# Kernel tuning notes

Measured on AMD Instinct MI355X. Metric: run time of the kernel, lower is better.

Reference implementation:

```python
import jax, jax.numpy as jnp
import numpy as np

B, N, D, H = 4, 2048, 512, 8
DH = D // H
EPS = 1e-6


def setup_inputs() -> dict:
    key = jax.random.key(0)
    ks = jax.random.split(key, 12)
    s = 1.0 / np.sqrt(D)
    return {
        "x": jax.random.normal(ks[0], (B, N, D), jnp.float32),
        "attn_bias": jax.random.normal(ks[1], (B, 1, N, N), jnp.float32),
        "Wq": jax.random.normal(ks[2], (D, D), jnp.float32) * s,
        "bq": jnp.zeros((D,), jnp.float32),
        "Wk": jax.random.normal(ks[3], (D, D), jnp.float32) * s,
        "bk": jnp.zeros((D,), jnp.float32),
        "Wv": jax.random.normal(ks[4], (D, D), jnp.float32) * s,
        "bv": jnp.zeros((D,), jnp.float32),
        "Wo": jax.random.normal(ks[5], (D, D), jnp.float32) * s,
        "bo": jnp.zeros((D,), jnp.float32),
        "q_gamma": jnp.ones((DH,), jnp.float32),
        "q_beta": jnp.zeros((DH,), jnp.float32),
        "k_gamma": jnp.ones((DH,), jnp.float32),
        "k_beta": jnp.zeros((DH,), jnp.float32),
    }


def _layernorm(x, gamma, beta):
    mu = jnp.mean(x, axis=-1, keepdims=True)
    var = jnp.var(x, axis=-1, keepdims=True)
    return (x - mu) * jax.lax.rsqrt(var + EPS) * gamma + beta


def reference(x, attn_bias, Wq, bq, Wk, bk, Wv, bv, Wo, bo,
              q_gamma, q_beta, k_gamma, k_beta):
    b, n, d = x.shape
    # project and split heads: (B, H, N, DH)
    def heads(W, bias):
        return (x @ W.T + bias).reshape(b, n, H, DH).transpose(0, 2, 1, 3)
    q = heads(Wq, bq)
    k = heads(Wk, bk)
    v = heads(Wv, bv)
    q = _layernorm(q, q_gamma, q_beta)
    k = _layernorm(k, k_gamma, k_beta)
    scores = jnp.einsum('bhqd,bhkd->bhqk', q, k) / np.sqrt(DH)
    scores = scores + attn_bias  # (B,1,N,N) broadcasts over heads
    attn = jax.nn.softmax(scores, axis=-1)
    out = jnp.einsum('bhqk,bhkd->bhqd', attn, v)
    out = out.transpose(0, 2, 1, 3).reshape(b, n, d)
    return out @ Wo.T + bo
```

## Files before the change

### kernel.cpp

```cpp
#include <hip/hip_runtime.h>

typedef __attribute__((ext_vector_type(8))) short short8;
typedef __attribute__((ext_vector_type(4))) float f32x4;
typedef __attribute__((ext_vector_type(4))) int i32x4;
typedef __attribute__((ext_vector_type(4))) unsigned short u16x4;
typedef __attribute__((ext_vector_type(2))) unsigned int u32x2;

#define B_  4
#define N_  2048
#define D_  512
#define H_  8
#define DH_ 64
#define M_  (B_ * N_)

__device__ __forceinline__ unsigned short f2bf(float f) {
    union { float f; unsigned u; } un; un.f = f;
    unsigned r = un.u + 0x7FFFu + ((un.u >> 16) & 1u);
    return (unsigned short)(r >> 16);
}
__device__ __forceinline__ float exp2fast(float x) {
#if __has_builtin(__builtin_amdgcn_exp2f)
    return __builtin_amdgcn_exp2f(x);
#else
    float r; asm("v_exp_f32 %0, %1" : "=v"(r) : "v"(x)); return r;
#endif
}
__device__ __forceinline__ unsigned cvtpk_bf16(float lo, float hi) {
    unsigned r;
    asm("v_cvt_pk_bf16_f32 %0, %1, %2" : "=v"(r) : "v"(lo), "v"(hi));
    return r;
}
__device__ __forceinline__ float max3f(float a, float b, float c) {
    return fmaxf(fmaxf(a, b), c);
}

typedef __attribute__((address_space(1))) const void gvoid;
typedef __attribute__((address_space(3))) void svoid;
__device__ __forceinline__ void load16_lds(const void* g, void* s) {
    __builtin_amdgcn_global_load_lds((gvoid*)g, (svoid*)s, 16, 0, 0);
}

__global__ __launch_bounds__(256) void cvt_all(
    const float* __restrict__ x,
    const float* __restrict__ W0, const float* __restrict__ W1,
    const float* __restrict__ W2, const float* __restrict__ W3,
    unsigned short* __restrict__ xb, unsigned short* __restrict__ Wb) {
    const int bx = blockIdx.x;
    const float* src;
    unsigned short* dst;
    int i;
    if (bx < 4096) {
        src = x; dst = xb;
        i = (bx * 256 + (int)threadIdx.x) * 4;
    } else {
        const int r = bx - 4096;
        const int sel = r >> 8;
        src = (sel == 0) ? W0 : (sel == 1) ? W1 : (sel == 2) ? W2 : W3;
        dst = Wb + (size_t)sel * D_ * D_;
        i = ((r & 255) * 256 + (int)threadIdx.x) * 4;
    }
    f32x4 v = *(const f32x4*)(src + i);
    u16x4 o;
    o[0] = f2bf(v[0]); o[1] = f2bf(v[1]); o[2] = f2bf(v[2]); o[3] = f2bf(v[3]);
    *(u16x4*)(dst + i) = o;
}

template <bool F32OUT, bool LNF>
__global__ __launch_bounds__(256, 2) void gemm_nt(
    const unsigned short* __restrict__ A,
    const unsigned short* __restrict__ W,
    const float* __restrict__ Bv0,
    const float* __restrict__ Bv1,
    const float* __restrict__ Bv2,
    const float* __restrict__ g0, const float* __restrict__ be0,
    const float* __restrict__ g1, const float* __restrict__ be1,
    unsigned short* __restrict__ outb,
    float* __restrict__ outf)
{
    const int mt = blockIdx.x;
    const int nt = blockIdx.y;
    const int sel = nt >> 2;
    const unsigned short* Wp = W + (size_t)sel * D_ * D_;
    const float* Bv = (sel == 0) ? Bv0 : (sel == 1) ? Bv1 : Bv2;
    const int n0 = (nt & 3) * 128;

    __shared__ __align__(16) unsigned short As[128 * 32];
    __shared__ __align__(16) unsigned short Bs[128 * 32];

    const int tid = threadIdx.x;
    const int w   = tid >> 6;
    const int l   = tid & 63;
    const int l15 = l & 15;
    const int qd  = l >> 4;
    const int wr  = w >> 1;
    const int wc  = w & 1;

    int srow[2], scol[2];
#pragma unroll
    for (int c = 0; c < 2; ++c) {
        const int g   = (w * 2 + c) * 64 + l;
        const int row = g >> 2;
        srow[c] = row;
        scol[c] = ((g & 3) ^ (row & 3)) * 8;
    }

    f32x4 acc[4][4];
#pragma unroll
    for (int i = 0; i < 4; ++i)
#pragma unroll
        for (int j = 0; j < 4; ++j)
            acc[i][j] = (f32x4){0.f, 0.f, 0.f, 0.f};

    const int swz = qd ^ (l15 & 3);

    for (int k0 = 0; k0 < D_; k0 += 32) {
        __syncthreads();
#pragma unroll
        for (int c = 0; c < 2; ++c) {
            load16_lds(A  + (size_t)(mt * 128 + srow[c]) * D_ + k0 + scol[c],
                       As + (w * 2 + c) * 512);
            load16_lds(Wp + (size_t)(n0 + srow[c]) * D_ + k0 + scol[c],
                       Bs + (w * 2 + c) * 512);
        }
        __syncthreads();

        short8 af[4], bfr[4];
#pragma unroll
        for (int rt = 0; rt < 4; ++rt)
            af[rt] = *(const short8*)&As[(wr * 64 + rt * 16 + l15) * 32 + swz * 8];
#pragma unroll
        for (int ct = 0; ct < 4; ++ct)
            bfr[ct] = *(const short8*)&Bs[(wc * 64 + ct * 16 + l15) * 32 + swz * 8];
#pragma unroll
        for (int rt = 0; rt < 4; ++rt)
#pragma unroll
            for (int ct = 0; ct < 4; ++ct)
                acc[rt][ct] = __builtin_amdgcn_mfma_f32_16x16x32_bf16(
                    af[rt], bfr[ct], acc[rt][ct], 0, 0, 0);
    }

    const float* gam = (sel == 0) ? g0 : g1;
    const float* bet = (sel == 0) ? be0 : be1;
    float gv[4], bv2[4];
    if (LNF) {
#pragma unroll
        for (int ct = 0; ct < 4; ++ct) { gv[ct] = gam[ct * 16 + l15]; bv2[ct] = bet[ct * 16 + l15]; }
    }

#pragma unroll
    for (int rt = 0; rt < 4; ++rt) {
        float v[4][4];
#pragma unroll
        for (int ct = 0; ct < 4; ++ct) {
            const float bias = Bv[n0 + wc * 64 + ct * 16 + l15];
#pragma unroll
            for (int r = 0; r < 4; ++r) v[ct][r] = acc[rt][ct][r] + bias;
        }
        if (LNF && sel < 2) {
#pragma unroll
            for (int r = 0; r < 4; ++r) {
                float s  = v[0][r] + v[1][r] + v[2][r] + v[3][r];
                float s2 = v[0][r]*v[0][r] + v[1][r]*v[1][r] + v[2][r]*v[2][r] + v[3][r]*v[3][r];
#pragma unroll
                for (int o = 1; o <= 8; o <<= 1) {
                    s  += __shfl_xor(s, o);
                    s2 += __shfl_xor(s2, o);
                }
                const float mu  = s * 0.015625f;
                const float var = s2 * 0.015625f - mu * mu;
                const float rs  = rsqrtf(var + 1e-6f);
#pragma unroll
                for (int ct = 0; ct < 4; ++ct)
                    v[ct][r] = (v[ct][r] - mu) * rs * gv[ct] + bv2[ct];
            }
        }
#pragma unroll
        for (int ct = 0; ct < 4; ++ct) {
            const int col  = n0 + wc * 64 + ct * 16 + l15;
            const int row0 = mt * 128 + wr * 64 + rt * 16 + qd * 4;
#pragma unroll
            for (int r = 0; r < 4; ++r) {
                const size_t oidx = (size_t)(row0 + r) * D_ + col;
                if (F32OUT) outf[oidx] = v[ct][r];
                else        outb[(size_t)sel * M_ * D_ + oidx] = f2bf(v[ct][r]);
            }
        }
    }
}

__global__ __launch_bounds__(256) void pack_kv(
    const unsigned short* __restrict__ K, const unsigned short* __restrict__ V,
    unsigned short* __restrict__ Kt, unsigned short* __restrict__ Vt2)
{
    const int nt = blockIdx.x, b = blockIdx.y;
    const int tid = threadIdx.x;
    __shared__ __align__(16) unsigned short Vl[64][520];

#pragma unroll
    for (int i = 0; i < 16; ++i) {
        const int c = i * 256 + tid;
        const int row = c >> 6, ch = c & 63;
        const size_t srow = ((size_t)(b * N_ + nt * 64 + row)) * D_ + ch * 8;
        i32x4 kd = *(const i32x4*)(K + srow);
        const int h = ch >> 3, dc = ch & 7;
        *(i32x4*)(Kt + ((((size_t)(b * 8 + h) * 32 + nt) * 64 + row) * 64) + dc * 8) = kd;
        i32x4 vd = *(const i32x4*)(V + srow);
        *(i32x4*)&Vl[row][ch * 8] = vd;
    }
    __syncthreads();
#pragma unroll
    for (int i = 0; i < 16; ++i) {
        const int c = i * 256 + tid;
        const int h = c >> 9, r = c & 511;
        const int dh = r >> 3, kc = r & 7;
        u16x4 o0, o1;
#pragma unroll
        for (int j = 0; j < 4; ++j) o0[j] = Vl[kc * 8 + j][h * 64 + dh];
#pragma unroll
        for (int j = 0; j < 4; ++j) o1[j] = Vl[kc * 8 + 4 + j][h * 64 + dh];
        const int t = kc >> 1;
        const int col0 = (t & 2) * 16 + (kc & 1) * 16 + (t & 1) * 4;
        const size_t rowbase = ((((size_t)(b * 8 + h) * 32 + nt) * 64 + dh) * 64);
        *(u16x4*)(Vt2 + rowbase + col0)     = o0;
        *(u16x4*)(Vt2 + rowbase + col0 + 8) = o1;
    }
}

__global__ __launch_bounds__(256, 2) void attn14(
    const unsigned short* __restrict__ Qm,
    const unsigned short* __restrict__ Kt,
    const unsigned short* __restrict__ Vt2,
    const float* __restrict__ Bias,
    unsigned short* __restrict__ AO)
{
    const int qt = blockIdx.x;
    const int h  = blockIdx.y;
    const int b  = blockIdx.z;
    const int w  = threadIdx.x >> 6;
    const int l  = threadIdx.x & 63;
    const int l15 = l & 15;
    const int qd  = l >> 4;
    const int q0 = qt * 128 + w * 32;
    const float L2E = 1.4426950408889634f;

    __shared__ __align__(16) unsigned char smem[16384];

    int soff[2], sc16[2];
#pragma unroll
    for (int i = 0; i < 2; ++i) {
        const int c = (w * 2 + i) * 64 + l;
        const int srow = c >> 3;
        const int sg   = (c & 7) ^ (srow & 7);
        soff[i] = srow * 64 + sg * 8;
        sc16[i] = c * 16;
    }

    short8 qf[2][2];
#pragma unroll
    for (int ct = 0; ct < 2; ++ct)
#pragma unroll
        for (int hf = 0; hf < 2; ++hf)
            qf[ct][hf] = *(const short8*)(Qm +
                (size_t)(b * N_ + q0 + ct * 16 + l15) * D_ + h * DH_ + hf * 32 + qd * 8);

    f32x4 Ot[4][2];
#pragma unroll
    for (int rt = 0; rt < 4; ++rt)
#pragma unroll
        for (int ct = 0; ct < 2; ++ct) Ot[rt][ct] = (f32x4){0.f, 0.f, 0.f, 0.f};
    float m_i[2] = {-3.0e38f, -3.0e38f};
    f32x4 li4[2];
    li4[0] = (f32x4){0.f, 0.f, 0.f, 0.f};
    li4[1] = (f32x4){0.f, 0.f, 0.f, 0.f};

    const unsigned short* Ktile0 = Kt  + (((size_t)(b * 8 + h) * 32) * 64) * 64;
    const unsigned short* Vtile0 = Vt2 + (((size_t)(b * 8 + h) * 32) * 64) * 64;
    const float* bQ0 = Bias + ((size_t)b * N_ + q0 + l15) * N_;
    const float* bQ1 = Bias + ((size_t)b * N_ + q0 + 16 + l15) * N_;

    load16_lds(Ktile0 + soff[0], smem + sc16[0]);
    load16_lds(Ktile0 + soff[1], smem + sc16[1]);

#define ATTN_ITER(KT, CUR) do {                                                \
    unsigned char* Kbc = smem + (CUR) * 8192;                                  \
    asm volatile("s_waitcnt vmcnt(0)" ::: "memory");                           \
    __builtin_amdgcn_s_barrier();                                              \
    __builtin_amdgcn_sched_barrier(0);                                         \
    f32x4 br[4][2];                                                            \
    _Pragma("unroll")                                                          \
    for (int rt = 0; rt < 4; ++rt) {                                           \
        br[rt][0] = *(const f32x4*)(bQ0 + (size_t)(KT) * 64 + rt * 16 + qd * 4); \
        br[rt][1] = *(const f32x4*)(bQ1 + (size_t)(KT) * 64 + rt * 16 + qd * 4); \
    }                                                                          \
    asm volatile("" ::: "memory");                    \
    short8 vf[4][2];                                                           \
    {                                                                          \
        const unsigned short* Vtl = Vtile0 + (size_t)(KT) * 4096;              \
        _Pragma("unroll")                                                      \
        for (int rt = 0; rt < 4; ++rt)                                         \
            _Pragma("unroll")                                                  \
            for (int hf = 0; hf < 2; ++hf)                                     \
                vf[rt][hf] = *(const short8*)(Vtl + (rt * 16 + l15) * 64 +     \
                                              hf * 32 + qd * 8);               \
    }                                                                          \
    asm volatile("" ::: "memory");                     \
    if ((KT) < 31) {                                                           \
        const unsigned short* Kn = Ktile0 + (size_t)((KT) + 1) * 4096;         \
        unsigned char* KbN = smem + (((CUR) ^ 1)) * 8192;                      \
        load16_lds(Kn + soff[0], KbN + sc16[0]);                               \
        load16_lds(Kn + soff[1], KbN + sc16[1]);                               \
    }                                                                          \
    asm volatile("" ::: "memory");                                             \
    short8 kf[4][2];                                                           \
    _Pragma("unroll")                                                          \
    for (int rt = 0; rt < 4; ++rt) {                                           \
        const int kv = rt * 16 + l15;                                          \
        _Pragma("unroll")                                                      \
        for (int hf = 0; hf < 2; ++hf) {                                       \
            const int cidx = (hf * 4 + qd) ^ (kv & 7);                         \
            kf[rt][hf] = *(const short8*)(Kbc + kv * 128 + cidx * 16);         \
        }                                                                      \
    }                                                                          \
    f32x4 St[4][2];                                                            \
    __builtin_amdgcn_s_setprio(1);                                             \
    _Pragma("unroll")                                                          \
    for (int rt = 0; rt < 4; ++rt)                                             \
        _Pragma("unroll")                                                      \
        for (int ct = 0; ct < 2; ++ct) {                                       \
            f32x4 v = (f32x4){0.f, 0.f, 0.f, 0.f};                             \
            v = __builtin_amdgcn_mfma_f32_16x16x32_bf16(kf[rt][0], qf[ct][0], v, 0, 0, 0); \
            v = __builtin_amdgcn_mfma_f32_16x16x32_bf16(kf[rt][1], qf[ct][1], v, 0, 0, 0); \
            St[rt][ct] = v;                                                    \
        }                                                                      \
    __builtin_amdgcn_s_setprio(0);                                             \
    _Pragma("unroll")                                                          \
    for (int ct = 0; ct < 2; ++ct) {                                           \
        f32x4 sv[4];                                                           \
        _Pragma("unroll")                                                      \
        for (int rt = 0; rt < 4; ++rt)                                         \
            sv[rt] = St[rt][ct] * 0.125f + br[rt][ct];                         \
        float mx0 = max3f(sv[0][0], sv[0][1], sv[0][2]);                       \
        float mx1 = max3f(sv[0][3], sv[1][0], sv[1][1]);                       \
        float mx2 = max3f(sv[1][2], sv[1][3], sv[2][0]);                       \
        float mx3 = max3f(sv[2][1], sv[2][2], sv[2][3]);                       \
        mx0 = max3f(mx0, sv[3][0], sv[3][1]);                                  \
        mx1 = max3f(mx1, sv[3][2], sv[3][3]);                                  \
        float mx = fmaxf(max3f(mx0, mx1, mx2), mx3);                           \
        mx = fmaxf(mx, __shfl_xor(mx, 16));                                    \
        mx = fmaxf(mx, __shfl_xor(mx, 32));                                    \
        if (__any(mx > m_i[ct] + 8.0f)) {                                      \
            const float mnew  = fmaxf(m_i[ct], mx);                            \
            const float alpha = exp2fast((m_i[ct] - mnew) * L2E);              \
            m_i[ct] = mnew;                                                    \
            li4[ct] *= alpha;                                                  \
            _Pragma("unroll")                                                  \
            for (int rt = 0; rt < 4; ++rt) Ot[rt][ct] *= alpha;                \
        }                                                                      \
        const float mL = m_i[ct] * L2E;                                        \
        f32x4 p[4];                                                            \
        _Pragma("unroll")                                                      \
        for (int rt = 0; rt < 4; ++rt) {                                       \
            f32x4 e = sv[rt] * L2E - mL;                                       \
            p[rt][0] = exp2fast(e[0]); p[rt][1] = exp2fast(e[1]);              \
            p[rt][2] = exp2fast(e[2]); p[rt][3] = exp2fast(e[3]);              \
        }                                                                      \
        li4[ct] += (p[0] + p[1]) + (p[2] + p[3]);                              \
        union { unsigned u[4]; short8 s; } pk0, pk1;                           \
        pk0.u[0] = cvtpk_bf16(p[0][0], p[0][1]);                               \
        pk0.u[1] = cvtpk_bf16(p[0][2], p[0][3]);                               \
        pk0.u[2] = cvtpk_bf16(p[1][0], p[1][1]);                               \
        pk0.u[3] = cvtpk_bf16(p[1][2], p[1][3]);                               \
        pk1.u[0] = cvtpk_bf16(p[2][0], p[2][1]);                               \
        pk1.u[1] = cvtpk_bf16(p[2][2], p[2][3]);                               \
        pk1.u[2] = cvtpk_bf16(p[3][0], p[3][1]);                               \
        pk1.u[3] = cvtpk_bf16(p[3][2], p[3][3]);                               \
        __builtin_amdgcn_s_setprio(1);                                         \
        _Pragma("unroll")                                                      \
        for (int rt = 0; rt < 4; ++rt) {                                       \
            Ot[rt][ct] = __builtin_amdgcn_mfma_f32_16x16x32_bf16(vf[rt][0], pk0.s, Ot[rt][ct], 0, 0, 0); \
            Ot[rt][ct] = __builtin_amdgcn_mfma_f32_16x16x32_bf16(vf[rt][1], pk1.s, Ot[rt][ct], 0, 0, 0); \
        }                                                                      \
        __builtin_amdgcn_s_setprio(0);                                         \
    }                                                                          \
} while (0)

    for (int kt2 = 0; kt2 < 16; ++kt2) {
        ATTN_ITER(kt2 * 2,     0);
        ATTN_ITER(kt2 * 2 + 1, 1);
    }
#undef ATTN_ITER

#pragma unroll
    for (int ct = 0; ct < 2; ++ct) {
        float l_i = (li4[ct][0] + li4[ct][1]) + (li4[ct][2] + li4[ct][3]);
        l_i += __shfl_xor(l_i, 16);
        l_i += __shfl_xor(l_i, 32);
        const float inv = 1.f / l_i;
        const int q = q0 + ct * 16 + l15;
#pragma unroll
        for (int rt = 0; rt < 4; ++rt) {
            u16x4 ob;
#pragma unroll
            for (int r = 0; r < 4; ++r) ob[r] = f2bf(Ot[rt][ct][r] * inv);
            *(u16x4*)(AO + (size_t)(b * N_ + q) * D_ + h * DH_ + rt * 16 + qd * 4) = ob;
        }
    }
}

extern "C" void kernel_launch(void* const* d_in, const int* in_sizes, int n_in,
                              void* d_out, int out_size, void* d_ws, size_t ws_size,
                              hipStream_t stream) {
    const float* x  = (const float*)d_in[0];
    const float* ab = (const float*)d_in[1];
    const float* Wq = (const float*)d_in[2];
    const float* bq = (const float*)d_in[3];
    const float* Wk = (const float*)d_in[4];
    const float* bk = (const float*)d_in[5];
    const float* Wv = (const float*)d_in[6];
    const float* bv = (const float*)d_in[7];
    const float* Wo = (const float*)d_in[8];
    const float* bo = (const float*)d_in[9];
    const float* qg = (const float*)d_in[10];
    const float* qb = (const float*)d_in[11];
    const float* kg = (const float*)d_in[12];
    const float* kb = (const float*)d_in[13];

    unsigned short* xb  = (unsigned short*)d_ws;
    unsigned short* Wb  = xb  + (size_t)M_ * D_;
    unsigned short* Y   = Wb  + (size_t)4 * D_ * D_;
    unsigned short* Kt  = Y   + (size_t)3 * M_ * D_;
    unsigned short* Vt2 = Kt  + (size_t)M_ * D_;
    unsigned short* AO  = Vt2 + (size_t)M_ * D_;
    float* out = (float*)d_out;

    cvt_all<<<dim3(5120), dim3(256), 0, stream>>>(x, Wq, Wk, Wv, Wo, xb, Wb);

    gemm_nt<false, true><<<dim3(64, 12), dim3(256), 0, stream>>>(
        xb, Wb, bq, bk, bv, qg, qb, kg, kb, Y, nullptr);

    pack_kv<<<dim3(32, 4), dim3(256), 0, stream>>>(
        Y + (size_t)M_ * D_, Y + (size_t)2 * M_ * D_, Kt, Vt2);

    attn14<<<dim3(16, 8, 4), dim3(256), 0, stream>>>(
        Y, Kt, Vt2, ab, AO);

    gemm_nt<true, false><<<dim3(64, 4), dim3(256), 0, stream>>>(
        AO, Wb + (size_t)3 * D_ * D_, bo, bo, bo,
        nullptr, nullptr, nullptr, nullptr, nullptr, out);
}
```

Baseline: 294.0 us.

## Fuse x fp32-to-bf16 conversion into QKV GEMM and stage V tiles in LDS

The separate conversion of x to bf16 is removed. The QKV GEMM now loads fp32 x directly, packs it to bf16 in registers and writes it to LDS, which saves a full activation round trip through global memory. The attention kernel moves to 512-thread blocks covering 256 queries and double-buffers both K and V tiles in LDS through async global-to-LDS loads, where V was previously read per-wave straight from global memory. The trade-offs are synchronous A-tile loads in the GEMM, which lose the async LDS copy, and larger LDS use per attention block, which may lower occupancy.

```diff
diff --git a/kernel.cpp b/kernel.cpp
--- a/kernel.cpp
+++ b/kernel.cpp
@@ -40,34 +40,25 @@
     __builtin_amdgcn_global_load_lds((gvoid*)g, (svoid*)s, 16, 0, 0);
 }
 
-__global__ __launch_bounds__(256) void cvt_all(
-    const float* __restrict__ x,
+__global__ __launch_bounds__(256) void cvt_w(
     const float* __restrict__ W0, const float* __restrict__ W1,
     const float* __restrict__ W2, const float* __restrict__ W3,
-    unsigned short* __restrict__ xb, unsigned short* __restrict__ Wb) {
+    unsigned short* __restrict__ Wb) {
     const int bx = blockIdx.x;
-    const float* src;
-    unsigned short* dst;
-    int i;
-    if (bx < 4096) {
-        src = x; dst = xb;
-        i = (bx * 256 + (int)threadIdx.x) * 4;
-    } else {
-        const int r = bx - 4096;
-        const int sel = r >> 8;
-        src = (sel == 0) ? W0 : (sel == 1) ? W1 : (sel == 2) ? W2 : W3;
-        dst = Wb + (size_t)sel * D_ * D_;
-        i = ((r & 255) * 256 + (int)threadIdx.x) * 4;
-    }
+    const int sel = bx >> 8;
+    const float* src = (sel == 0) ? W0 : (sel == 1) ? W1 : (sel == 2) ? W2 : W3;
+    unsigned short* dst = Wb + (size_t)sel * D_ * D_;
+    const int i = ((bx & 255) * 256 + (int)threadIdx.x) * 4;
     f32x4 v = *(const f32x4*)(src + i);
     u16x4 o;
     o[0] = f2bf(v[0]); o[1] = f2bf(v[1]); o[2] = f2bf(v[2]); o[3] = f2bf(v[3]);
     *(u16x4*)(dst + i) = o;
 }
 
-template <bool F32OUT, bool LNF>
+template <bool AF32, bool F32OUT, bool LNF>
 __global__ __launch_bounds__(256, 2) void gemm_nt(
     const unsigned short* __restrict__ A,
+    const float* __restrict__ Af,
     const unsigned short* __restrict__ W,
     const float* __restrict__ Bv0,
     const float* __restrict__ Bv1,
@@ -117,8 +108,21 @@
         __syncthreads();
 #pragma unroll
         for (int c = 0; c < 2; ++c) {
-            load16_lds(A  + (size_t)(mt * 128 + srow[c]) * D_ + k0 + scol[c],
-                       As + (w * 2 + c) * 512);
+            if (AF32) {
+                const int g = (w * 2 + c) * 64 + l;
+                const float* srcA = Af + (size_t)(mt * 128 + srow[c]) * D_ + k0 + scol[c];
+                f32x4 v0 = *(const f32x4*)srcA;
+                f32x4 v1 = *(const f32x4*)(srcA + 4);
+                union { unsigned u[4]; short8 s; } pk;
+                pk.u[0] = cvtpk_bf16(v0[0], v0[1]);
+                pk.u[1] = cvtpk_bf16(v0[2], v0[3]);
+                pk.u[2] = cvtpk_bf16(v1[0], v1[1]);
+                pk.u[3] = cvtpk_bf16(v1[2], v1[3]);
+                *(short8*)&As[g * 8] = pk.s;
+            } else {
+                load16_lds(A + (size_t)(mt * 128 + srow[c]) * D_ + k0 + scol[c],
+                           As + (w * 2 + c) * 512);
+            }
             load16_lds(Wp + (size_t)(n0 + srow[c]) * D_ + k0 + scol[c],
                        Bs + (w * 2 + c) * 512);
         }
@@ -226,7 +230,7 @@
     }
 }
 
-__global__ __launch_bounds__(256, 2) void attn14(
+__global__ __launch_bounds__(512, 2) void attn16(
     const unsigned short* __restrict__ Qm,
     const unsigned short* __restrict__ Kt,
     const unsigned short* __restrict__ Vt2,
@@ -240,20 +244,16 @@
     const int l  = threadIdx.x & 63;
     const int l15 = l & 15;
     const int qd  = l >> 4;
-    const int q0 = qt * 128 + w * 32;
+    const int q0 = qt * 256 + w * 32;
     const float L2E = 1.4426950408889634f;
 
-    __shared__ __align__(16) unsigned char smem[16384];
-
-    int soff[2], sc16[2];
-#pragma unroll
-    for (int i = 0; i < 2; ++i) {
-        const int c = (w * 2 + i) * 64 + l;
-        const int srow = c >> 3;
-        const int sg   = (c & 7) ^ (srow & 7);
-        soff[i] = srow * 64 + sg * 8;
-        sc16[i] = c * 16;
-    }
+    __shared__ __align__(16) unsigned char smem[32768];
+
+    const int c    = w * 64 + l;
+    const int srow = c >> 3;
+    const int sg   = (c & 7) ^ (srow & 7);
+    const int soff = srow * 64 + sg * 8;
+    const int sc16 = c * 16;
 
     short8 qf[2][2];
 #pragma unroll
@@ -278,11 +278,12 @@
     const float* bQ0 = Bias + ((size_t)b * N_ + q0 + l15) * N_;
     const float* bQ1 = Bias + ((size_t)b * N_ + q0 + 16 + l15) * N_;
 
-    load16_lds(Ktile0 + soff[0], smem + sc16[0]);
-    load16_lds(Ktile0 + soff[1], smem + sc16[1]);
+    load16_lds(Ktile0 + soff, smem + sc16);
+    load16_lds(Vtile0 + soff, smem + 8192 + sc16);
 
 #define ATTN_ITER(KT, CUR) do {                                                \
-    unsigned char* Kbc = smem + (CUR) * 8192;                                  \
+    unsigned char* Kbc = smem + (CUR) * 16384;                                 \
+    unsigned char* Vbc = Kbc + 8192;                                           \
     asm volatile("s_waitcnt vmcnt(0)" ::: "memory");                           \
     __builtin_amdgcn_s_barrier();                                              \
     __builtin_amdgcn_sched_barrier(0);                                         \
@@ -292,23 +293,13 @@
         br[rt][0] = *(const f32x4*)(bQ0 + (size_t)(KT) * 64 + rt * 16 + qd * 4); \
         br[rt][1] = *(const f32x4*)(bQ1 + (size_t)(KT) * 64 + rt * 16 + qd * 4); \
     }                                                                          \
-    asm volatile("" ::: "memory");                    \
-    short8 vf[4][2];                                                           \
-    {                                                                          \
-        const unsigned short* Vtl = Vtile0 + (size_t)(KT) * 4096;              \
-        _Pragma("unroll")                                                      \
-        for (int rt = 0; rt < 4; ++rt)                                         \
-            _Pragma("unroll")                                                  \
-            for (int hf = 0; hf < 2; ++hf)                                     \
-                vf[rt][hf] = *(const short8*)(Vtl + (rt * 16 + l15) * 64 +     \
-                                              hf * 32 + qd * 8);               \
-    }                                                                          \
-    asm volatile("" ::: "memory");                     \
+    asm volatile("" ::: "memory");                   \
     if ((KT) < 31) {                                                           \
         const unsigned short* Kn = Ktile0 + (size_t)((KT) + 1) * 4096;         \
-        unsigned char* KbN = smem + (((CUR) ^ 1)) * 8192;                      \
-        load16_lds(Kn + soff[0], KbN + sc16[0]);                               \
-        load16_lds(Kn + soff[1], KbN + sc16[1]);                               \
+        const unsigned short* Vn = Vtile0 + (size_t)((KT) + 1) * 4096;         \
+        unsigned char* KbN = smem + (((CUR) ^ 1)) * 16384;                     \
+        load16_lds(Kn + soff, KbN + sc16);                                     \
+        load16_lds(Vn + soff, KbN + 8192 + sc16);                              \
     }                                                                          \
     asm volatile("" ::: "memory");                                             \
     short8 kf[4][2];                                                           \
@@ -333,6 +324,16 @@
             St[rt][ct] = v;                                                    \
         }                                                                      \
     __builtin_amdgcn_s_setprio(0);                                             \
+    short8 vf[4][2];                                                           \
+    _Pragma("unroll")                                                          \
+    for (int rt = 0; rt < 4; ++rt) {                                           \
+        const int dh = rt * 16 + l15;                                          \
+        _Pragma("unroll")                                                      \
+        for (int hf = 0; hf < 2; ++hf) {                                       \
+            const int cidx = (hf * 4 + qd) ^ (dh & 7);                         \
+            vf[rt][hf] = *(const short8*)(Vbc + dh * 128 + cidx * 16);         \
+        }                                                                      \
+    }                                                                          \
     _Pragma("unroll")                                                          \
     for (int ct = 0; ct < 2; ++ct) {                                           \
         f32x4 sv[4];                                                           \
@@ -425,26 +426,25 @@
     const float* kg = (const float*)d_in[12];
     const float* kb = (const float*)d_in[13];
 
-    unsigned short* xb  = (unsigned short*)d_ws;
-    unsigned short* Wb  = xb  + (size_t)M_ * D_;
+    unsigned short* Wb  = (unsigned short*)d_ws;
     unsigned short* Y   = Wb  + (size_t)4 * D_ * D_;
     unsigned short* Kt  = Y   + (size_t)3 * M_ * D_;
     unsigned short* Vt2 = Kt  + (size_t)M_ * D_;
     unsigned short* AO  = Vt2 + (size_t)M_ * D_;
     float* out = (float*)d_out;
 
-    cvt_all<<<dim3(5120), dim3(256), 0, stream>>>(x, Wq, Wk, Wv, Wo, xb, Wb);
-
-    gemm_nt<false, true><<<dim3(64, 12), dim3(256), 0, stream>>>(
-        xb, Wb, bq, bk, bv, qg, qb, kg, kb, Y, nullptr);
+    cvt_w<<<dim3(1024), dim3(256), 0, stream>>>(Wq, Wk, Wv, Wo, Wb);
+
+    gemm_nt<true, false, true><<<dim3(64, 12), dim3(256), 0, stream>>>(
+        nullptr, x, Wb, bq, bk, bv, qg, qb, kg, kb, Y, nullptr);
 
     pack_kv<<<dim3(32, 4), dim3(256), 0, stream>>>(
         Y + (size_t)M_ * D_, Y + (size_t)2 * M_ * D_, Kt, Vt2);
 
-    attn14<<<dim3(16, 8, 4), dim3(256), 0, stream>>>(
+    attn16<<<dim3(8, 8, 4), dim3(512), 0, stream>>>(
         Y, Kt, Vt2, ab, AO);
 
-    gemm_nt<true, false><<<dim3(64, 4), dim3(256), 0, stream>>>(
-        AO, Wb + (size_t)3 * D_ * D_, bo, bo, bo,
+    gemm_nt<false, true, false><<<dim3(64, 4), dim3(256), 0, stream>>>(
+        AO, nullptr, Wb + (size_t)3 * D_ * D_, bo, bo, bo,
         nullptr, nullptr, nullptr, nullptr, nullptr, out);
 }
```

New measurement: 272.7 us. -7.3%, faster.
